# Kernel optimization log

Hardware: AMD Instinct MI355X
Metric: run time of the kernel (lower is better)

## Reference

```python
import jax, jax.numpy as jnp
import numpy as np

NEG_SLOPE = 0.2
EPS = 1e-16


def _gat_conv(x, src, dst, edge_attr, W, We, att_src, att_dst, att_edge, bias):
    """PyG GATConv, heads=H, concat=False, edge_dim given. x:[N,F_in]."""
    N = x.shape[0]
    H, C = att_src.shape
    xs = (x @ W.T).reshape(N, H, C)                      # [N,H,C]
    a_src = jnp.einsum('nhc,hc->nh', xs, att_src)        # [N,H]
    a_dst = jnp.einsum('nhc,hc->nh', xs, att_dst)        # [N,H]
    e = (edge_attr @ We.T).reshape(-1, H, C)             # [E,H,C]
    a_edge = jnp.einsum('ehc,hc->eh', e, att_edge)       # [E,H]
    alpha = a_src[src] + a_dst[dst] + a_edge             # [E,H]
    alpha = jax.nn.leaky_relu(alpha, NEG_SLOPE)
    # segment softmax over destination nodes (per head)
    amax = jax.ops.segment_max(alpha, dst, num_segments=N)   # [N,H]
    ex = jnp.exp(alpha - amax[dst])
    denom = jax.ops.segment_sum(ex, dst, num_segments=N)     # [N,H]
    alpha = ex / (denom[dst] + EPS)
    msg = xs[src] * alpha[..., None]                     # [E,H,C]
    out = jax.ops.segment_sum(msg, dst, num_segments=N)  # [N,H,C]
    return out.mean(axis=1) + bias                       # concat=False -> mean over heads


def _add_self_loops(src, dst, edge_attr, N):
    # PyG add_self_loops with fill_value='mean': per-dst mean of incoming edge_attr
    ones = jnp.ones((edge_attr.shape[0],), edge_attr.dtype)
    sums = jax.ops.segment_sum(edge_attr, dst, num_segments=N)
    cnt = jax.ops.segment_sum(ones, dst, num_segments=N)
    loop_attr = sums / jnp.maximum(cnt, 1.0)[:, None]
    idx = jnp.arange(N, dtype=src.dtype)
    return (jnp.concatenate([src, idx]), jnp.concatenate([dst, idx]),
            jnp.concatenate([edge_attr, loop_attr], axis=0))


def setup_inputs() -> dict:
    key = jax.random.key(0)
    ks = jax.random.split(key, 16)
    N, E, F_IN, C, H = 100000, 1600000, 64, 32, 4
    s = 0.1
    inp = {
        'x': jax.random.normal(ks[0], (N, F_IN), jnp.float32),
        'edge_index': jax.random.randint(ks[1], (2, E), 0, N, jnp.int32),
        'edge_weight': jax.random.uniform(ks[2], (E, 1), jnp.float32),
        'w1': jax.random.normal(ks[3], (H * C, F_IN), jnp.float32) * s,
        'we1': jax.random.normal(ks[4], (H * C, 1), jnp.float32) * s,
        'as1': jax.random.normal(ks[5], (H, C), jnp.float32) * s,
        'ad1': jax.random.normal(ks[6], (H, C), jnp.float32) * s,
        'ae1': jax.random.normal(ks[7], (H, C), jnp.float32) * s,
        'b1': jnp.zeros((C,), jnp.float32),
        'w2': jax.random.normal(ks[8], (H * C, C), jnp.float32) * s,
        'we2': jax.random.normal(ks[9], (H * C, 1), jnp.float32) * s,
        'as2': jax.random.normal(ks[10], (H, C), jnp.float32) * s,
        'ad2': jax.random.normal(ks[11], (H, C), jnp.float32) * s,
        'ae2': jax.random.normal(ks[12], (H, C), jnp.float32) * s,
        'b2': jnp.zeros((C,), jnp.float32),
    }
    return inp


def reference(x, edge_index, edge_weight, w1, we1, as1, ad1, ae1, b1,
              w2, we2, as2, ad2, ae2, b2):
    N = x.shape[0]
    src, dst, ea = _add_self_loops(edge_index[0], edge_index[1], edge_weight, N)
    h = jax.nn.relu(_gat_conv(x, src, dst, ea, w1, we1, as1, ad1, ae1, b1))
    # nn.Dropout is identity in eval mode
    h = jax.nn.relu(_gat_conv(h, src, dst, ea, w2, we2, as2, ad2, ae2, b2))
    return h
```

## Files before the change

kernel.cpp:

```cpp
#include <hip/hip_runtime.h>
#include <hip/hip_fp16.h>
#include <cstddef>

#define GAT_EPS 1e-16f
#define CAP 48
#define SRC_MASK 0xFFFFFu
#define EA_SCALE 4096.0f

__global__ __launch_bounds__(256, 2)
void k_gemm1h(const float* __restrict__ x, const float* __restrict__ W,
              const float* __restrict__ as_, const float* __restrict__ ad_,
              __half* __restrict__ xs, float* __restrict__ asrc,
              float* __restrict__ adst, int N, int gemmb,
              const int* __restrict__ src, const int* __restrict__ dst,
              const float* __restrict__ ew, int* __restrict__ cnt,
              unsigned* __restrict__ epk, int E,
              const float* __restrict__ we1, const float* __restrict__ ae1,
              const float* __restrict__ we2, const float* __restrict__ ae2,
              float* __restrict__ wd,
              const float* __restrict__ as2, const float* __restrict__ ad2,
              const float* __restrict__ W2, float* __restrict__ vs2,
              float* __restrict__ vd2) {
    if (blockIdx.x == gridDim.x - 1) {
        int t = threadIdx.x;
        if (t < 128) {
            float v1 = we1[t] * ae1[t];
            float v2 = we2[t] * ae2[t];
#pragma unroll
            for (int off = 16; off; off >>= 1) {
                v1 += __shfl_xor(v1, off);
                v2 += __shfl_xor(v2, off);
            }
            if ((t & 31) == 0) { wd[t >> 5] = v1; wd[4 + (t >> 5)] = v2; }
            int h = t >> 5, c = t & 31;
            float s = 0.f, dv = 0.f;
            for (int k = 0; k < 32; k++) {
                float w = W2[(h * 32 + k) * 32 + c];
                s  += as2[h * 32 + k] * w;
                dv += ad2[h * 32 + k] * w;
            }
            vs2[t] = s;
            vd2[t] = dv;
        }
        return;
    }
    int g = blockIdx.x / 5;
    int r = blockIdx.x % 5;
    if (r != 0) {
        int i = (g * 4 + r - 1) * 256 + threadIdx.x;
        if (i < E) {
            int d = dst[i];
            int p = atomicAdd(&cnt[d], 1);
            p = min(p, CAP - 1);
            unsigned qe = (unsigned)fminf(ew[i] * EA_SCALE + 0.5f, 4095.0f);
            epk[(size_t)d * CAP + p] = (qe << 20) | ((unsigned)src[i] & SRC_MASK);
        }
        return;
    }
    if (g >= gemmb) return;

    int n0 = g * 64;
    int t = threadIdx.x;
    int tx = t & 31;
    int ty = t >> 5;
    __shared__ __half Wh[64 * 132];
    __shared__ float xsh[64 * 65];
    int nrows = min(64, N - n0);
    for (int j = t; j < 8192; j += 256) {
        int c = j >> 6, k = j & 63;
        Wh[k * 132 + ((c & 31) << 2) + (c >> 5)] = __float2half(W[j]);
    }
    const float* xg = x + (size_t)n0 * 64;
    for (int j = t; j < nrows * 64; j += 256) xsh[(j >> 6) * 65 + (j & 63)] = xg[j];
    __syncthreads();

    float acc[8][4];
#pragma unroll
    for (int i = 0; i < 8; i++)
#pragma unroll
        for (int j = 0; j < 4; j++) acc[i][j] = 0.f;

#pragma unroll 4
    for (int k = 0; k < 64; k++) {
        const __half2* wp = reinterpret_cast<const __half2*>(&Wh[k * 132 + (tx << 2)]);
        float2 wf0 = __half22float2(wp[0]);
        float2 wf1 = __half22float2(wp[1]);
#pragma unroll
        for (int i = 0; i < 8; i++) {
            float xv = xsh[(ty * 8 + i) * 65 + k];
            acc[i][0] += xv * wf0.x;
            acc[i][1] += xv * wf0.y;
            acc[i][2] += xv * wf1.x;
            acc[i][3] += xv * wf1.y;
        }
    }

    float asv[4], adv[4];
#pragma unroll
    for (int j = 0; j < 4; j++) { asv[j] = as_[32 * j + tx]; adv[j] = ad_[32 * j + tx]; }

#pragma unroll
    for (int i = 0; i < 8; i++) {
        int row = ty * 8 + i;
        bool ok = row < nrows;
        __half* orow = xs + (size_t)(n0 + row) * 128;
#pragma unroll
        for (int j = 0; j < 4; j++) {
            if (ok) orow[32 * j + tx] = __float2half(acc[i][j]);
            float vs = acc[i][j] * asv[j];
            float vd = acc[i][j] * adv[j];
#pragma unroll
            for (int off = 16; off; off >>= 1) {
                vs += __shfl_xor(vs, off);
                vd += __shfl_xor(vd, off);
            }
            if (ok && tx == 0) {
                asrc[(size_t)(n0 + row) * 4 + j] = vs;
                adst[(size_t)(n0 + row) * 4 + j] = vd;
            }
        }
    }
}

__global__ void k_gather1(const unsigned* __restrict__ epk, const int* __restrict__ cnt,
                          const __half* __restrict__ xs,
                          const float* __restrict__ asrc, const float* __restrict__ adst,
                          const float* __restrict__ wedot, const float* __restrict__ bias,
                          const float* __restrict__ vs2, const float* __restrict__ vd2,
                          __half2* __restrict__ h1, float* __restrict__ asrc2,
                          float* __restrict__ adst2, int N) {
    int node = blockIdx.x * 4 + (threadIdx.x >> 6);
    if (node >= N) return;
    int l = threadIdx.x & 63;
    int q = l >> 4;
    int p = l & 15;
    int h = p >> 2;
    float wd = wedot[h];
    float ad = adst[(size_t)node * 4 + h];
    int cv = min(cnt[node], CAP);
    int beg = node * CAP;
    int end = beg + cv;

    float a0 = 0.f, a1 = 0.f, a2 = 0.f, a3 = 0.f;
    float a4 = 0.f, a5 = 0.f, a6 = 0.f, a7 = 0.f, ds = 0.f, easum = 0.f;
#pragma unroll 2
    for (int i = beg; i < end; i += 4) {
        int idx = i + q;
        bool valid = idx < end;
        unsigned e = epk[valid ? idx : end - 1];
        int s = (int)(e & SRC_MASK);
        float ea = (float)(e >> 20) * (1.0f / EA_SCALE);
        easum += valid ? ea : 0.f;
        float as = asrc[(size_t)s * 4 + h];
        float al = as + ad + ea * wd;
        al = fmaxf(al, 0.2f * al);
        float w = valid ? __expf(al) : 0.f;
        uint4 raw = reinterpret_cast<const uint4*>(xs + (size_t)s * 128)[p];
        const __half2* hp = reinterpret_cast<const __half2*>(&raw);
        float2 f0 = __half22float2(hp[0]);
        float2 f1 = __half22float2(hp[1]);
        float2 f2 = __half22float2(hp[2]);
        float2 f3 = __half22float2(hp[3]);
        a0 += w * f0.x; a1 += w * f0.y;
        a2 += w * f1.x; a3 += w * f1.y;
        a4 += w * f2.x; a5 += w * f2.y;
        a6 += w * f3.x; a7 += w * f3.y;
        ds += w;
    }
    easum += __shfl_xor(easum, 16);
    easum += __shfl_xor(easum, 32);
    float loop_ea = easum / fmaxf((float)cv, 1.0f);
    float aln = asrc[(size_t)node * 4 + h] + ad + loop_ea * wd;
    aln = fmaxf(aln, 0.2f * aln);
    float wl = __expf(aln);
    if (q == 0) {
        uint4 raw = reinterpret_cast<const uint4*>(xs + (size_t)node * 128)[p];
        const __half2* hp = reinterpret_cast<const __half2*>(&raw);
        float2 f0 = __half22float2(hp[0]);
        float2 f1 = __half22float2(hp[1]);
        float2 f2 = __half22float2(hp[2]);
        float2 f3 = __half22float2(hp[3]);
        a0 += wl * f0.x; a1 += wl * f0.y;
        a2 += wl * f1.x; a3 += wl * f1.y;
        a4 += wl * f2.x; a5 += wl * f2.y;
        a6 += wl * f3.x; a7 += wl * f3.y;
        ds += wl;
    }
    a0 += __shfl_xor(a0, 16); a1 += __shfl_xor(a1, 16);
    a2 += __shfl_xor(a2, 16); a3 += __shfl_xor(a3, 16);
    a4 += __shfl_xor(a4, 16); a5 += __shfl_xor(a5, 16);
    a6 += __shfl_xor(a6, 16); a7 += __shfl_xor(a7, 16);
    ds += __shfl_xor(ds, 16);
    a0 += __shfl_xor(a0, 32); a1 += __shfl_xor(a1, 32);
    a2 += __shfl_xor(a2, 32); a3 += __shfl_xor(a3, 32);
    a4 += __shfl_xor(a4, 32); a5 += __shfl_xor(a5, 32);
    a6 += __shfl_xor(a6, 32); a7 += __shfl_xor(a7, 32);
    ds += __shfl_xor(ds, 32);
    float inv = 1.f / (ds + GAT_EPS);
    a0 *= inv; a1 *= inv; a2 *= inv; a3 *= inv;
    a4 *= inv; a5 *= inv; a6 *= inv; a7 *= inv;
    a0 += __shfl_xor(a0, 4); a1 += __shfl_xor(a1, 4);
    a2 += __shfl_xor(a2, 4); a3 += __shfl_xor(a3, 4);
    a4 += __shfl_xor(a4, 4); a5 += __shfl_xor(a5, 4);
    a6 += __shfl_xor(a6, 4); a7 += __shfl_xor(a7, 4);
    a0 += __shfl_xor(a0, 8); a1 += __shfl_xor(a1, 8);
    a2 += __shfl_xor(a2, 8); a3 += __shfl_xor(a3, 8);
    a4 += __shfl_xor(a4, 8); a5 += __shfl_xor(a5, 8);
    a6 += __shfl_xor(a6, 8); a7 += __shfl_xor(a7, 8);
    if (l < 4) {
        int c0 = l * 8;
        float rv[8];
        rv[0] = fmaxf(0.25f * a0 + bias[c0 + 0], 0.f);
        rv[1] = fmaxf(0.25f * a1 + bias[c0 + 1], 0.f);
        rv[2] = fmaxf(0.25f * a2 + bias[c0 + 2], 0.f);
        rv[3] = fmaxf(0.25f * a3 + bias[c0 + 3], 0.f);
        rv[4] = fmaxf(0.25f * a4 + bias[c0 + 4], 0.f);
        rv[5] = fmaxf(0.25f * a5 + bias[c0 + 5], 0.f);
        rv[6] = fmaxf(0.25f * a6 + bias[c0 + 6], 0.f);
        rv[7] = fmaxf(0.25f * a7 + bias[c0 + 7], 0.f);
        __half2* hp = h1 + (size_t)node * 16 + l * 4;
        hp[0] = __floats2half2_rn(rv[0], rv[1]);
        hp[1] = __floats2half2_rn(rv[2], rv[3]);
        hp[2] = __floats2half2_rn(rv[4], rv[5]);
        hp[3] = __floats2half2_rn(rv[6], rv[7]);
        float pa[4] = {0.f, 0.f, 0.f, 0.f}, pd[4] = {0.f, 0.f, 0.f, 0.f};
#pragma unroll
        for (int hh = 0; hh < 4; hh++)
#pragma unroll
            for (int j = 0; j < 8; j++) {
                pa[hh] += rv[j] * vs2[hh * 32 + c0 + j];
                pd[hh] += rv[j] * vd2[hh * 32 + c0 + j];
            }
#pragma unroll
        for (int hh = 0; hh < 4; hh++) {
            pa[hh] += __shfl_xor(pa[hh], 1);
            pa[hh] += __shfl_xor(pa[hh], 2);
            pd[hh] += __shfl_xor(pd[hh], 1);
            pd[hh] += __shfl_xor(pd[hh], 2);
        }
        if (l == 0) {
            float4 wa, wb;
            wa.x = pa[0]; wa.y = pa[1]; wa.z = pa[2]; wa.w = pa[3];
            wb.x = pd[0]; wb.y = pd[1]; wb.z = pd[2]; wb.w = pd[3];
            *reinterpret_cast<float4*>(asrc2 + (size_t)node * 4) = wa;
            *reinterpret_cast<float4*>(adst2 + (size_t)node * 4) = wb;
        }
    }
}

__global__ void k_gather2(const unsigned* __restrict__ epk, const int* __restrict__ cnt,
                          const __half* __restrict__ h1,
                          const float* __restrict__ asrc, const float* __restrict__ adst,
                          const float* __restrict__ wedot, const float* __restrict__ W2,
                          const float* __restrict__ bias, float* __restrict__ out, int N) {
    __shared__ float W2sh[128 * 33];
    __shared__ float Ash[4][128];
    int t = threadIdx.x;
    for (int j = t; j < 4096; j += 256) {
        int hh = j >> 10, k = (j >> 5) & 31, c = j & 31;
        W2sh[(hh * 32 + c) * 33 + k] = W2[j];
    }
    __syncthreads();

    int node0 = blockIdx.x * 4 + (t >> 6);
    bool live = node0 < N;
    int node = live ? node0 : 0;
    int l = t & 63;
    int q = l >> 4;
    int g = l & 15;
    int h = g >> 2;
    int j4 = g & 3;
    float wd = wedot[h];
    float ad = adst[(size_t)node * 4 + h];
    int cv = min(cnt[node], CAP);
    int beg = node * CAP;
    int end = beg + cv;

    float A0 = 0.f, A1 = 0.f, A2 = 0.f, A3 = 0.f;
    float A4 = 0.f, A5 = 0.f, A6 = 0.f, A7 = 0.f;
    float ds = 0.f, easum = 0.f;
#pragma unroll 2
    for (int i = beg; i < end; i += 4) {
        int idx = i + q;
        bool valid = idx < end;
        unsigned e = epk[valid ? idx : end - 1];
        int s = (int)(e & SRC_MASK);
        float ea = (float)(e >> 20) * (1.0f / EA_SCALE);
        easum += valid ? ea : 0.f;
        float as = asrc[(size_t)s * 4 + h];
        float al = as + ad + ea * wd;
        al = fmaxf(al, 0.2f * al);
        float w = valid ? __expf(al) : 0.f;
        uint4 raw = reinterpret_cast<const uint4*>(h1 + (size_t)s * 32)[j4];
        const __half2* hp = reinterpret_cast<const __half2*>(&raw);
        float2 f0 = __half22float2(hp[0]);
        float2 f1 = __half22float2(hp[1]);
        float2 f2 = __half22float2(hp[2]);
        float2 f3 = __half22float2(hp[3]);
        A0 += w * f0.x; A1 += w * f0.y;
        A2 += w * f1.x; A3 += w * f1.y;
        A4 += w * f2.x; A5 += w * f2.y;
        A6 += w * f3.x; A7 += w * f3.y;
        ds += w;
    }
    easum += __shfl_xor(easum, 16);
    easum += __shfl_xor(easum, 32);
    float loop_ea = easum / fmaxf((float)cv, 1.0f);
    float aln = asrc[(size_t)node * 4 + h] + ad + loop_ea * wd;
    aln = fmaxf(aln, 0.2f * aln);
    float wl = __expf(aln);
    if (q == 0) {
        uint4 raw = reinterpret_cast<const uint4*>(h1 + (size_t)node * 32)[j4];
        const __half2* hp = reinterpret_cast<const __half2*>(&raw);
        float2 f0 = __half22float2(hp[0]);
        float2 f1 = __half22float2(hp[1]);
        float2 f2 = __half22float2(hp[2]);
        float2 f3 = __half22float2(hp[3]);
        A0 += wl * f0.x; A1 += wl * f0.y;
        A2 += wl * f1.x; A3 += wl * f1.y;
        A4 += wl * f2.x; A5 += wl * f2.y;
        A6 += wl * f3.x; A7 += wl * f3.y;
        ds += wl;
    }
    A0 += __shfl_xor(A0, 16); A1 += __shfl_xor(A1, 16);
    A2 += __shfl_xor(A2, 16); A3 += __shfl_xor(A3, 16);
    A4 += __shfl_xor(A4, 16); A5 += __shfl_xor(A5, 16);
    A6 += __shfl_xor(A6, 16); A7 += __shfl_xor(A7, 16);
    ds += __shfl_xor(ds, 16);
    A0 += __shfl_xor(A0, 32); A1 += __shfl_xor(A1, 32);
    A2 += __shfl_xor(A2, 32); A3 += __shfl_xor(A3, 32);
    A4 += __shfl_xor(A4, 32); A5 += __shfl_xor(A5, 32);
    A6 += __shfl_xor(A6, 32); A7 += __shfl_xor(A7, 32);
    ds += __shfl_xor(ds, 32);
    float inv = 1.f / (ds + GAT_EPS);
    if (q == 0) {
        float* ap = &Ash[t >> 6][h * 32 + j4 * 8];
        ap[0] = A0 * inv; ap[1] = A1 * inv; ap[2] = A2 * inv; ap[3] = A3 * inv;
        ap[4] = A4 * inv; ap[5] = A5 * inv; ap[6] = A6 * inv; ap[7] = A7 * inv;
    }
    __syncthreads();
    int k = l & 31;
    int hp2 = l >> 5;
    const float* arow = Ash[t >> 6];
    float part = 0.f;
#pragma unroll
    for (int hh = 2 * hp2; hh <= 2 * hp2 + 1; hh++) {
        const float* wrow = &W2sh[(hh * 32) * 33 + k];
#pragma unroll 8
        for (int c = 0; c < 32; c++)
            part += arow[hh * 32 + c] * wrow[c * 33];
    }
    part += __shfl_xor(part, 32);
    if (live && l < 32)
        out[(size_t)node * 32 + k] = fmaxf(0.25f * part + bias[k], 0.f);
}

extern "C" void kernel_launch(void* const* d_in, const int* in_sizes, int n_in,
                              void* d_out, int out_size, void* d_ws, size_t ws_size,
                              hipStream_t stream) {
    const float* x   = (const float*)d_in[0];
    const int*   ei  = (const int*)d_in[1];
    const float* ewt = (const float*)d_in[2];
    const float* w1  = (const float*)d_in[3];
    const float* we1 = (const float*)d_in[4];
    const float* as1 = (const float*)d_in[5];
    const float* ad1 = (const float*)d_in[6];
    const float* ae1 = (const float*)d_in[7];
    const float* b1  = (const float*)d_in[8];
    const float* w2  = (const float*)d_in[9];
    const float* we2 = (const float*)d_in[10];
    const float* as2 = (const float*)d_in[11];
    const float* ad2 = (const float*)d_in[12];
    const float* ae2 = (const float*)d_in[13];
    const float* b2  = (const float*)d_in[14];

    const int N = in_sizes[0] / 64;
    const int E = in_sizes[1] / 2;
    const int* srcI = ei;
    const int* dstI = ei + E;

    char* base = (char*)d_ws;
    size_t off = 0;
    auto alloc = [&](size_t bytes) { char* p = base + off; off += (bytes + 15) & ~(size_t)15; return p; };
    __half* xs     = (__half*)alloc((size_t)N * 128 * sizeof(__half));
    __half2* h1    = (__half2*)alloc((size_t)N * 16 * sizeof(__half2));
    float* asrc    = (float*)alloc((size_t)N * 4 * sizeof(float));
    float* adst    = (float*)alloc((size_t)N * 4 * sizeof(float));
    float* asrc2   = (float*)alloc((size_t)N * 4 * sizeof(float));
    float* adst2   = (float*)alloc((size_t)N * 4 * sizeof(float));
    int*   cnt     = (int*)alloc((size_t)N * sizeof(int));
    unsigned* epk  = (unsigned*)alloc((size_t)N * CAP * sizeof(unsigned));
    float* wedot   = (float*)alloc(8 * sizeof(float));
    float* vs2     = (float*)alloc(128 * sizeof(float));
    float* vd2     = (float*)alloc(128 * sizeof(float));

    float* outF = (float*)d_out;

    hipMemsetAsync(cnt, 0, (size_t)N * sizeof(int), stream);

    const int gemmb = (N + 63) / 64;
    const int histb = (E + 255) / 256;
    const int G = gemmb > (histb + 3) / 4 ? gemmb : (histb + 3) / 4;
    const int gb = (N + 3) / 4;

    k_gemm1h<<<5 * G + 1, 256, 0, stream>>>(x, w1, as1, ad1, xs, asrc, adst, N, gemmb,
                                            srcI, dstI, ewt, cnt, epk, E,
                                            we1, ae1, we2, ae2, wedot,
                                            as2, ad2, w2, vs2, vd2);

    k_gather1<<<gb, 256, 0, stream>>>(epk, cnt, xs, asrc, adst,
                                      wedot + 0, b1, vs2, vd2, h1, asrc2, adst2, N);

    k_gather2<<<gb, 256, 0, stream>>>(epk, cnt, (const __half*)h1, asrc2, adst2,
                                      wedot + 4, w2, b2, outF, N);
}
```

Baseline: 303.1 us.

## Replace global-atomic edge bucketing with two-pass shared-memory radix binning

Edge insertion into per-node slot lists no longer does one global atomicAdd per edge. It now bins edges by destination bucket of 512 nodes using a block histogram, a scan and a scatter into a temporary binned array. A final per-bucket kernel fills the per-node lists with shared-memory atomics and writes the counts directly, which also drops the large memset. The GEMM blocks are regrouped alongside the scatter blocks. This trades contended global atomics and random writes for two extra kernel launches and an extra pass over an E-sized int2 buffer.

```diff
diff --git a/kernel.cpp b/kernel.cpp
--- a/kernel.cpp
+++ b/kernel.cpp
@@ -6,23 +6,56 @@
 #define CAP 48
 #define SRC_MASK 0xFFFFFu
 #define EA_SCALE 4096.0f
+#define EPB 4096
+
+__global__ void k_binA(const int* __restrict__ dst, int* __restrict__ blockbase,
+                       int* __restrict__ bucket_cnt, int E) {
+    __shared__ int hist[256];
+    int t = threadIdx.x;
+    hist[t] = 0;
+    __syncthreads();
+    int base = blockIdx.x * EPB;
+#pragma unroll
+    for (int j = 0; j < 16; j++) {
+        int i = base + j * 256 + t;
+        if (i < E) atomicAdd(&hist[dst[i] >> 9], 1);
+    }
+    __syncthreads();
+    blockbase[blockIdx.x * 256 + t] = atomicAdd(&bucket_cnt[t], hist[t]);
+}
+
+__global__ void k_scan(const int* __restrict__ bucket_cnt, int* __restrict__ bucket_base) {
+    __shared__ int sh[256];
+    int t = threadIdx.x;
+    int v = bucket_cnt[t];
+    sh[t] = v;
+    __syncthreads();
+    for (int off = 1; off < 256; off <<= 1) {
+        int u = (t >= off) ? sh[t - off] : 0;
+        __syncthreads();
+        sh[t] += u;
+        __syncthreads();
+    }
+    bucket_base[t] = sh[t] - v;
+    if (t == 255) bucket_base[256] = sh[255];
+}
 
 __global__ __launch_bounds__(256, 2)
-void k_gemm1h(const float* __restrict__ x, const float* __restrict__ W,
-              const float* __restrict__ as_, const float* __restrict__ ad_,
-              __half* __restrict__ xs, float* __restrict__ asrc,
-              float* __restrict__ adst, int N, int gemmb,
-              const int* __restrict__ src, const int* __restrict__ dst,
-              const float* __restrict__ ew, int* __restrict__ cnt,
-              unsigned* __restrict__ epk, int E,
-              const float* __restrict__ we1, const float* __restrict__ ae1,
-              const float* __restrict__ we2, const float* __restrict__ ae2,
-              float* __restrict__ wd,
-              const float* __restrict__ as2, const float* __restrict__ ad2,
-              const float* __restrict__ W2, float* __restrict__ vs2,
-              float* __restrict__ vd2) {
+void k_binB(const int* __restrict__ src, const int* __restrict__ dst,
+            const float* __restrict__ ew, const int* __restrict__ blockbase,
+            const int* __restrict__ bucket_base, int2* __restrict__ binned, int E,
+            const float* __restrict__ x, const float* __restrict__ W,
+            const float* __restrict__ as_, const float* __restrict__ ad_,
+            __half* __restrict__ xs, float* __restrict__ asrc,
+            float* __restrict__ adst, int N, int gemmb,
+            const float* __restrict__ we1, const float* __restrict__ ae1,
+            const float* __restrict__ we2, const float* __restrict__ ae2,
+            float* __restrict__ wd,
+            const float* __restrict__ as2, const float* __restrict__ ad2,
+            const float* __restrict__ W2, float* __restrict__ vs2,
+            float* __restrict__ vd2) {
+    int t = threadIdx.x;
     if (blockIdx.x == gridDim.x - 1) {
-        int t = threadIdx.x;
         if (t < 128) {
             float v1 = we1[t] * ae1[t];
             float v2 = we2[t] * ae2[t];
@@ -46,21 +79,30 @@
     }
     int g = blockIdx.x / 5;
     int r = blockIdx.x % 5;
-    if (r != 0) {
-        int i = (g * 4 + r - 1) * 256 + threadIdx.x;
-        if (i < E) {
-            int d = dst[i];
-            int p = atomicAdd(&cnt[d], 1);
-            p = min(p, CAP - 1);
-            unsigned qe = (unsigned)fminf(ew[i] * EA_SCALE + 0.5f, 4095.0f);
-            epk[(size_t)d * CAP + p] = (qe << 20) | ((unsigned)src[i] & SRC_MASK);
+    if (r == 0) {
+        __shared__ int lcnt[256];
+        lcnt[t] = bucket_base[t] + blockbase[g * 256 + t];
+        __syncthreads();
+        int base = g * EPB;
+#pragma unroll
+        for (int j = 0; j < 16; j++) {
+            int i = base + j * 256 + t;
+            if (i < E) {
+                int d = dst[i];
+                int p = atomicAdd(&lcnt[d >> 9], 1);
+                unsigned qe = (unsigned)fminf(ew[i] * EA_SCALE + 0.5f, 4095.0f);
+                int2 en;
+                en.x = (int)((qe << 20) | ((unsigned)src[i] & SRC_MASK));
+                en.y = d;
+                binned[p] = en;
+            }
         }
         return;
     }
-    if (g >= gemmb) return;
-
-    int n0 = g * 64;
-    int t = threadIdx.x;
+    int gi = g * 4 + r - 1;
+    if (gi >= gemmb) return;
+
+    int n0 = gi * 64;
     int tx = t & 31;
     int ty = t >> 5;
     __shared__ __half Wh[64 * 132];
@@ -120,6 +162,28 @@
             }
         }
     }
+}
+
+__global__ void k_binC(const int2* __restrict__ binned, const int* __restrict__ bucket_base,
+                       int* __restrict__ cnt, unsigned* __restrict__ epk, int N) {
+    __shared__ int lcnt[512];
+    int t = threadIdx.x;
+    lcnt[t] = 0;
+    lcnt[t + 256] = 0;
+    __syncthreads();
+    int b = blockIdx.x;
+    int beg = bucket_base[b], end = bucket_base[b + 1];
+    for (int i = beg + t; i < end; i += 256) {
+        int2 e = binned[i];
+        int d = e.y;
+        int p = atomicAdd(&lcnt[d & 511], 1);
+        if (p < CAP) epk[(size_t)d * CAP + p] = (unsigned)e.x;
+    }
+    __syncthreads();
+    int d0 = (b << 9) + t;
+    if (d0 < N) cnt[d0] = lcnt[t];
+    int d1 = (b << 9) + 256 + t;
+    if (d1 < N) cnt[d1] = lcnt[t + 256];
 }
 
 __global__ void k_gather1(const unsigned* __restrict__ epk, const int* __restrict__ cnt,
@@ -390,23 +454,33 @@
     float* adst2   = (float*)alloc((size_t)N * 4 * sizeof(float));
     int*   cnt     = (int*)alloc((size_t)N * sizeof(int));
     unsigned* epk  = (unsigned*)alloc((size_t)N * CAP * sizeof(unsigned));
+    int2*  binned  = (int2*)alloc((size_t)E * sizeof(int2));
     float* wedot   = (float*)alloc(8 * sizeof(float));
     float* vs2     = (float*)alloc(128 * sizeof(float));
     float* vd2     = (float*)alloc(128 * sizeof(float));
+    int*   bucket_cnt  = (int*)alloc(256 * sizeof(int));
+    int*   bucket_base = (int*)alloc(257 * sizeof(int));
+
+    const int binb  = (E + EPB - 1) / EPB;
+    int*   blockbase = (int*)alloc((size_t)binb * 256 * sizeof(int));
 
     float* outF = (float*)d_out;
 
-    hipMemsetAsync(cnt, 0, (size_t)N * sizeof(int), stream);
+    hipMemsetAsync(bucket_cnt, 0, 256 * sizeof(int), stream);
 
     const int gemmb = (N + 63) / 64;
-    const int histb = (E + 255) / 256;
-    const int G = gemmb > (histb + 3) / 4 ? gemmb : (histb + 3) / 4;
+    const int gpb = (gemmb + 3) / 4;
+    const int G = binb > gpb ? binb : gpb;
     const int gb = (N + 3) / 4;
-
-    k_gemm1h<<<5 * G + 1, 256, 0, stream>>>(x, w1, as1, ad1, xs, asrc, adst, N, gemmb,
-                                            srcI, dstI, ewt, cnt, epk, E,
-                                            we1, ae1, we2, ae2, wedot,
-                                            as2, ad2, w2, vs2, vd2);
+    const int nbuckets = (N + 511) >> 9;
+
+    k_binA<<<binb, 256, 0, stream>>>(dstI, blockbase, bucket_cnt, E);
+    k_scan<<<1, 256, 0, stream>>>(bucket_cnt, bucket_base);
+    k_binB<<<5 * G + 1, 256, 0, stream>>>(srcI, dstI, ewt, blockbase, bucket_base,
+                                          binned, E, x, w1, as1, ad1, xs, asrc, adst,
+                                          N, gemmb, we1, ae1, we2, ae2, wedot,
+                                          as2, ad2, w2, vs2, vd2);
+    k_binC<<<nbuckets, 256, 0, stream>>>(binned, bucket_base, cnt, epk, N);
 
     k_gather1<<<gb, 256, 0, stream>>>(epk, cnt, xs, asrc, adst,
                                       wedot + 0, b1, vs2, vd2, h1, asrc2, adst2, N);
```

New measurement: 286.3 us, median of 2. 5.5% less time.
